# Optimization experiments

Measured on AMD Instinct MI355X. Metric: run time of the kernel, lower is better.

Reference implementation:

```python
import jax, jax.numpy as jnp
import numpy as np

B, C, N, M = 4, 192, 160, 160
HEADS, DH = 4, 32
HID = HEADS * DH
NMEM = 4
SCALE = DH ** -0.5


def setup_inputs() -> dict:
    key = jax.random.key(0)
    ks = jax.random.split(key, 8)
    std = 0.05
    return {
        "x": jax.random.normal(ks[0], (B, C, N, M), jnp.float32),
        "gq": jnp.ones((C,), jnp.float32),
        "gk": jnp.ones((C,), jnp.float32),
        "gv": jnp.ones((C,), jnp.float32),
        "Wq": jax.random.normal(ks[1], (HID, C), jnp.float32) * std,
        "Wk": jax.random.normal(ks[2], (HID, C), jnp.float32) * std,
        "Wv": jax.random.normal(ks[3], (HID, C), jnp.float32) * std,
        "mem_kv": jax.random.normal(ks[4], (2, HEADS, NMEM, DH), jnp.float32),
        "Wo": jax.random.normal(ks[5], (C, HID), jnp.float32) * std,
        "bo": jnp.zeros((C,), jnp.float32),
        "Wr": jax.random.normal(ks[6], (C, 2 * C), jnp.float32) * std,
    }


def _rms(x, g):
    # lucidrains RMSNorm over channel axis 1: F.normalize(x, dim=1) * g * sqrt(dim)
    n = jnp.sqrt(jnp.sum(x * x, axis=1, keepdims=True))
    gshape = (1, -1) + (1,) * (x.ndim - 2)
    return x / jnp.maximum(n, 1e-12) * g.reshape(gshape) * jnp.sqrt(jnp.asarray(x.shape[1], x.dtype))


def _axial_attn(q_ft, k_ft, v_map, rep, Wq, Wk, Wv, mem_kv, Wo, bo, gq, gk, gv):
    # q_ft: (b, c, Lq) compact queries (spatial (1,Lq) in the original)
    # k_ft: (b, c, Lk) compact keys; original repeats them `rep` times -> (Lk*rep) keys
    # v_map: (b, c, Lk, rep) values (full map, not broadcast)
    # Exact math of softmax over [NMEM + Lk*rep] keys, exploiting the rep-fold
    # duplicated key scores so attn(key i, copy j) has identical weight p_i:
    #   out = sum_mem p_j mem_v_j + sum_i p_i * (sum_rep v[i, r])
    b = q_ft.shape[0]
    q = jnp.einsum('hdc,bcq->bhqd', Wq.reshape(HEADS, DH, -1), _rms(q_ft, gq))
    k = jnp.einsum('hdc,bck->bhkd', Wk.reshape(HEADS, DH, -1), _rms(k_ft, gk))
    v = jnp.einsum('hdc,bckr->bhkrd', Wv.reshape(HEADS, DH, -1), _rms(v_map, gv))
    v_sum = v.sum(axis=3)  # (b,h,Lk,d)
    mem_k, mem_v = mem_kv[0], mem_kv[1]
    s_k = jnp.einsum('bhqd,bhkd->bhqk', q, k) * SCALE      # (b,h,Lq,Lk)
    s_m = jnp.einsum('bhqd,hjd->bhqj', q, mem_k) * SCALE   # (b,h,Lq,NMEM)
    mx = jnp.maximum(s_k.max(-1), s_m.max(-1))             # (b,h,Lq)
    e_k = jnp.exp(s_k - mx[..., None])
    e_m = jnp.exp(s_m - mx[..., None])
    Z = e_m.sum(-1) + rep * e_k.sum(-1)                    # rep copies of each key
    out = (jnp.einsum('bhqj,hjd->bhqd', e_m, mem_v)
           + jnp.einsum('bhqk,bhkd->bhqd', e_k, v_sum)) / Z[..., None]
    out = out.transpose(0, 2, 1, 3).reshape(b, -1, HID)    # (b,Lq,hid), (h d) channel order
    return jnp.einsum('ck,bqk->bcq', Wo, out) + bo[None, :, None]  # (b,c,Lq)


def reference(x, gq, gk, gv, Wq, Wk, Wv, mem_kv, Wo, bo, Wr):
    # x: (b,c,n,m); mask=None path
    row_ft = x.mean(axis=3)  # (b,c,n)
    col_ft = x.mean(axis=2)  # (b,c,m)
    # row attention: n queries, keys = col_ft repeated n times, values = x^T (spatial (m,n))
    row_attn = _axial_attn(row_ft, col_ft, x.transpose(0, 1, 3, 2), N,
                           Wq, Wk, Wv, mem_kv, Wo, bo, gq, gk, gv)  # (b,c,n)
    # col attention (shared weights): m queries, keys = row_ft repeated m times, values = x
    col_attn = _axial_attn(col_ft, row_ft, x, M,
                           Wq, Wk, Wv, mem_kv, Wo, bo, gq, gk, gv)  # (b,c,m)
    # broadcast to (b,c,n,m), concat on channels, 1x1 conv reduce (bias=False)
    Wr1, Wr2 = Wr[:, :C], Wr[:, C:]
    out = (jnp.einsum('dc,bcn->bdn', Wr1, row_attn)[:, :, :, None]
           + jnp.einsum('dc,bcm->bdm', Wr2, col_attn)[:, :, None, :])
    return out
```

## Files before the change

kernel.cpp:

```cpp
#include <hip/hip_runtime.h>
#include <math.h>

constexpr int B_ = 4, C_ = 192, N_ = 160, M_ = 160;
constexpr int NM_ = N_ * M_;
constexpr float SQRT_C = 13.856406460551018f;
constexpr float SCALE_ = 0.17677669529663687f;

__device__ __forceinline__ float wred_sum(float v) {
    #pragma unroll
    for (int o = 32; o > 0; o >>= 1) v += __shfl_xor(v, o, 64);
    return v;
}
__device__ __forceinline__ float wred_max(float v) {
    #pragma unroll
    for (int o = 32; o > 0; o >>= 1) v = fmaxf(v, __shfl_xor(v, o, 64));
    return v;
}

__global__ __launch_bounds__(256) void mega1_kernel(
        const float* __restrict__ x,
        const float* __restrict__ Wr, const float* __restrict__ Wo,
        const float* __restrict__ bo,
        const float* __restrict__ Wq, const float* __restrict__ Wk,
        const float* __restrict__ Wv, const float* __restrict__ gq,
        const float* __restrict__ gk, const float* __restrict__ gv,
        float* __restrict__ rn,
        float* __restrict__ rowft, float* __restrict__ colft,
        float* __restrict__ WfT2, float* __restrict__ bfb,
        float* __restrict__ WT) {
    __shared__ float4 sp4[4][64];
    __shared__ float cpart[4][160];
    int bx = blockIdx.x, tid = threadIdx.x;
    int w = tid >> 6, lane = tid & 63;
    if (bx < 400) {
        int g4 = bx * 64 + lane;
        int b = g4 / 6400, nm4 = g4 - b * 6400;
        const float* xb = x + (size_t)b * (C_ * NM_) + (size_t)nm4 * 4
                            + (size_t)(w * 48) * NM_;
        float4 s = make_float4(0.f, 0.f, 0.f, 0.f);
        #pragma unroll 16
        for (int cc = 0; cc < 48; cc++) {
            float4 v = *reinterpret_cast<const float4*>(xb + (size_t)cc * NM_);
            s.x += v.x * v.x; s.y += v.y * v.y; s.z += v.z * v.z; s.w += v.w * v.w;
        }
        sp4[w][lane] = s;
        __syncthreads();
        if (tid < 64) {
            float4 a = sp4[0][tid], b2 = sp4[1][tid], c2 = sp4[2][tid], d2 = sp4[3][tid];
            float4 r;
            r.x = SQRT_C / fmaxf(sqrtf(a.x + b2.x + c2.x + d2.x), 1e-12f);
            r.y = SQRT_C / fmaxf(sqrtf(a.y + b2.y + c2.y + d2.y), 1e-12f);
            r.z = SQRT_C / fmaxf(sqrtf(a.z + b2.z + c2.z + d2.z), 1e-12f);
            r.w = SQRT_C / fmaxf(sqrtf(a.w + b2.w + c2.w + d2.w), 1e-12f);
            *reinterpret_cast<float4*>(rn + (size_t)(bx * 64 + tid) * 4) = r;
        }
    } else if (bx < 1168) {
        int bc = bx - 400;
        const float* xp = x + (size_t)bc * NM_;
        bool act = (lane < 40);
        float4 cs = make_float4(0.f, 0.f, 0.f, 0.f);
        for (int n = w; n < N_; n += 4) {
            float4 v = act ? *reinterpret_cast<const float4*>(xp + n * M_ + lane * 4)
                           : make_float4(0.f, 0.f, 0.f, 0.f);
            cs.x += v.x; cs.y += v.y; cs.z += v.z; cs.w += v.w;
            float rs = wred_sum(v.x + v.y + v.z + v.w);
            if (lane == 0) rowft[bc * N_ + n] = rs * (1.0f / 160.0f);
        }
        if (act) {
            cpart[w][lane * 4 + 0] = cs.x; cpart[w][lane * 4 + 1] = cs.y;
            cpart[w][lane * 4 + 2] = cs.z; cpart[w][lane * 4 + 3] = cs.w;
        }
        __syncthreads();
        if (tid < 160) {
            float sr = cpart[0][tid] + cpart[1][tid] + cpart[2][tid] + cpart[3][tid];
            colft[bc * M_ + tid] = sr * (1.0f / 160.0f);
        }
    } else if (bx < 1360) {
        int pair = (bx - 1168) * 2 + (tid >> 7);
        int hd = tid & 127;
        int t = pair / 192, dch = pair % 192;
        const float* wr = Wr + dch * 384 + t * 192;
        float acc = 0.f;
        for (int c = 0; c < 192; c++) acc += wr[c] * Wo[c * 128 + hd];
        WfT2[pair * 128 + hd] = acc;
        if (hd == 0) {
            float sb = 0.f;
            for (int c = 0; c < 192; c++) sb += wr[c] * bo[c];
            bfb[pair] = sb;
        }
    } else {
        int g = (bx - 1360) * 256 + tid;
        int mat = g / 24576, r2 = g - mat * 24576;
        const float* W  = (mat == 0) ? Wq : ((mat == 1) ? Wk : Wv);
        const float* gp = (mat == 0) ? gq : ((mat == 1) ? gk : gv);
        WT[g] = gp[r2 % 192] * W[r2];
    }
}

__global__ __launch_bounds__(512) void sweighted_kernel(
        const float* __restrict__ x, const float* __restrict__ rn,
        float* __restrict__ Srow, float* __restrict__ Scol) {
    __shared__ float cpart[8][160];
    int bc = blockIdx.x;
    int b = bc / C_;
    int tid = threadIdx.x, w = tid >> 6, lane = tid & 63;
    const float* xp = x + (size_t)bc * NM_;
    const float* rp = rn + (size_t)b * NM_;
    bool act = (lane < 40);
    float4 acc = make_float4(0.f, 0.f, 0.f, 0.f);
    for (int n = w; n < N_; n += 8) {
        float4 xv = act ? *reinterpret_cast<const float4*>(xp + n * M_ + lane * 4)
                        : make_float4(0.f, 0.f, 0.f, 0.f);
        float4 rv = act ? *reinterpret_cast<const float4*>(rp + n * M_ + lane * 4)
                        : make_float4(0.f, 0.f, 0.f, 0.f);
        float4 p;
        p.x = xv.x * rv.x; p.y = xv.y * rv.y; p.z = xv.z * rv.z; p.w = xv.w * rv.w;
        acc.x += p.x; acc.y += p.y; acc.z += p.z; acc.w += p.w;
        float rs = wred_sum(p.x + p.y + p.z + p.w);
        if (lane == 0) Srow[bc * N_ + n] = rs;
    }
    if (act) {
        cpart[w][lane * 4 + 0] = acc.x; cpart[w][lane * 4 + 1] = acc.y;
        cpart[w][lane * 4 + 2] = acc.z; cpart[w][lane * 4 + 3] = acc.w;
    }
    __syncthreads();
    if (tid < 160) {
        float sn = 0.f;
        #pragma unroll
        for (int ww = 0; ww < 8; ww++) sn += cpart[ww][tid];
        Scol[bc * M_ + tid] = sn;
    }
}

__global__ __launch_bounds__(256) void proj_kernel(
        const float* __restrict__ WT,
        const float* __restrict__ rowft, const float* __restrict__ colft,
        const float* __restrict__ Srow, const float* __restrict__ Scol,
        float* __restrict__ Qb, float* __restrict__ Kb, float* __restrict__ Vb) {
    __shared__ float in_s[4 * 196];
    __shared__ float sc_s[4];
    int bx = blockIdx.x;
    int pt = bx % 40, rest = bx / 40;
    int mat = rest % 3; int r2 = rest / 3;
    int t = r2 % 2, b = r2 / 2;
    const float* src; float* dst;
    if (mat == 0)      { src = (t == 0) ? rowft : colft; dst = Qb; }
    else if (mat == 1) { src = (t == 0) ? colft : rowft; dst = Kb; }
    else               { src = (t == 0) ? Scol  : Srow;  dst = Vb; }
    const float* Wt = WT + mat * 24576;
    int tid = threadIdx.x;
    for (int idx = tid; idx < 768; idx += 256) {
        int c = idx >> 2, p = idx & 3;
        in_s[p * 196 + c] = src[(b * C_ + c) * 160 + pt * 4 + p];
    }
    __syncthreads();
    int w = tid >> 6, lane = tid & 63;
    if (mat < 2) {
        float v0 = in_s[w * 196 + lane];
        float v1 = in_s[w * 196 + lane + 64];
        float v2 = in_s[w * 196 + lane + 128];
        float ssq = wred_sum(v0 * v0 + v1 * v1 + v2 * v2);
        if (lane == 0) sc_s[w] = SQRT_C / fmaxf(sqrtf(ssq), 1e-12f);
    } else {
        if (tid < 4) sc_s[tid] = 1.0f;
    }
    __syncthreads();
    int hd = tid & 127, p0 = (tid >> 7) * 2;
    const float* wp = Wt + hd * 192;
    const float* i0p = &in_s[p0 * 196];
    const float* i1p = &in_s[(p0 + 1) * 196];
    float a0 = 0.f, a1 = 0.f;
    #pragma unroll 4
    for (int c0 = 0; c0 < 192; c0 += 4) {
        float4 wv = *reinterpret_cast<const float4*>(wp + c0);
        float4 u0 = *reinterpret_cast<const float4*>(i0p + c0);
        float4 u1 = *reinterpret_cast<const float4*>(i1p + c0);
        a0 += wv.x * u0.x + wv.y * u0.y + wv.z * u0.z + wv.w * u0.w;
        a1 += wv.x * u1.x + wv.y * u1.y + wv.z * u1.z + wv.w * u1.w;
    }
    int posbase = (b * 2 + t) * 160 + pt * 4 + p0;
    dst[(size_t)posbase * 128 + hd]       = a0 * sc_s[p0];
    dst[(size_t)(posbase + 1) * 128 + hd] = a1 * sc_s[p0 + 1];
}

__global__ __launch_bounds__(256) void attn_kernel(
        const float* __restrict__ Qb, const float* __restrict__ Kb,
        const float* __restrict__ Vb, const float* __restrict__ memkv,
        float* __restrict__ AO) {
    __shared__ float k_s[160 * 36];
    __shared__ float v_s[32 * 172];
    __shared__ float q_s[8 * 36];
    __shared__ float e_s[8 * 160];
    __shared__ float mk[128];
    __shared__ float mv[128];
    int bx = blockIdx.x;
    int qt = bx % 20; int r = bx / 20;
    int h = r & 3; r >>= 2;
    int t = r & 1; int b = r >> 1;
    int tid = threadIdx.x, w = tid >> 6, lane = tid & 63;
    int btbase = ((b * 2 + t) * 160) * 128 + h * 32;
    for (int idx = tid; idx < 1280; idx += 256) {
        int k = idx >> 3, dq = idx & 7;
        float4 kv = *reinterpret_cast<const float4*>(Kb + btbase + k * 128 + dq * 4);
        *reinterpret_cast<float4*>(&k_s[k * 36 + dq * 4]) = kv;
        float4 vv = *reinterpret_cast<const float4*>(Vb + btbase + k * 128 + dq * 4);
        v_s[(dq * 4 + 0) * 172 + k] = vv.x;
        v_s[(dq * 4 + 1) * 172 + k] = vv.y;
        v_s[(dq * 4 + 2) * 172 + k] = vv.z;
        v_s[(dq * 4 + 3) * 172 + k] = vv.w;
    }
    if (tid < 64) {
        int q = tid >> 3, dq = tid & 7;
        *reinterpret_cast<float4*>(&q_s[q * 36 + dq * 4]) =
            *reinterpret_cast<const float4*>(Qb + btbase + (qt * 8 + q) * 128 + dq * 4);
    }
    if (tid < 128) {
        mk[tid] = memkv[h * 128 + tid];
        mv[tid] = memkv[512 + h * 128 + tid];
    }
    __syncthreads();
    float4 kr0[8], kr1[8], kr2[8];
    #pragma unroll
    for (int dq = 0; dq < 8; dq++) {
        kr0[dq] = *reinterpret_cast<const float4*>(&k_s[lane * 36 + dq * 4]);
        kr1[dq] = *reinterpret_cast<const float4*>(&k_s[(lane + 64) * 36 + dq * 4]);
        if (lane < 32) kr2[dq] = *reinterpret_cast<const float4*>(&k_s[(lane + 128) * 36 + dq * 4]);
        else           kr2[dq] = make_float4(0.f, 0.f, 0.f, 0.f);
    }
    float p;
    {
        int pj = lane >> 3, qi = pj >> 2, j = pj & 3;
        int db = (lane & 7) * 4;
        float4 qv = *reinterpret_cast<const float4*>(&q_s[(w * 2 + qi) * 36 + db]);
        float4 mkv = *reinterpret_cast<const float4*>(&mk[j * 32 + db]);
        p = qv.x * mkv.x + qv.y * mkv.y + qv.z * mkv.z + qv.w * mkv.w;
        p += __shfl_xor(p, 1, 64); p += __shfl_xor(p, 2, 64); p += __shfl_xor(p, 4, 64);
        p *= SCALE_;
    }
    float sm[2][4];
    #pragma unroll
    for (int j = 0; j < 4; j++) {
        sm[0][j] = __shfl(p, j * 8, 64);
        sm[1][j] = __shfl(p, 32 + j * 8, 64);
    }
    int dpv = lane & 31;
    float Zq[2], accm[2];
    #pragma unroll
    for (int qi = 0; qi < 2; qi++) {
        const float* qrow = &q_s[(w * 2 + qi) * 36];
        float s0 = 0.f, s1 = 0.f, s2 = 0.f;
        #pragma unroll
        for (int dq = 0; dq < 8; dq++) {
            float4 qv = *reinterpret_cast<const float4*>(qrow + dq * 4);
            s0 += qv.x * kr0[dq].x + qv.y * kr0[dq].y + qv.z * kr0[dq].z + qv.w * kr0[dq].w;
            s1 += qv.x * kr1[dq].x + qv.y * kr1[dq].y + qv.z * kr1[dq].z + qv.w * kr1[dq].w;
            s2 += qv.x * kr2[dq].x + qv.y * kr2[dq].y + qv.z * kr2[dq].z + qv.w * kr2[dq].w;
        }
        s0 *= SCALE_; s1 *= SCALE_;
        s2 = (lane < 32) ? s2 * SCALE_ : -1e30f;
        float mx = fmaxf(fmaxf(s0, s1), s2);
        mx = fmaxf(mx, fmaxf(fmaxf(sm[qi][0], sm[qi][1]), fmaxf(sm[qi][2], sm[qi][3])));
        mx = wred_max(mx);
        float e0 = __expf(s0 - mx), e1 = __expf(s1 - mx);
        float e2 = (lane < 32) ? __expf(s2 - mx) : 0.f;
        int eb = (w * 2 + qi) * 160;
        e_s[eb + lane] = e0; e_s[eb + 64 + lane] = e1;
        if (lane < 32) e_s[eb + 128 + lane] = e2;
        float esum = wred_sum(e0 + e1 + e2);
        float em0 = __expf(sm[qi][0] - mx), em1 = __expf(sm[qi][1] - mx);
        float em2 = __expf(sm[qi][2] - mx), em3 = __expf(sm[qi][3] - mx);
        Zq[qi] = (em0 + em1 + em2 + em3) + 160.0f * esum;
        accm[qi] = em0 * mv[dpv] + em1 * mv[32 + dpv] + em2 * mv[64 + dpv] + em3 * mv[96 + dpv];
    }
    int half = lane >> 5, k0 = half * 80;
    const float* vrow = &v_s[dpv * 172 + k0];
    const float* e0p = &e_s[(w * 2) * 160 + k0];
    const float* e1p = &e_s[(w * 2 + 1) * 160 + k0];
    float a0 = 0.f, a1 = 0.f;
    #pragma unroll 4
    for (int kk = 0; kk < 80; kk += 4) {
        float4 vv = *reinterpret_cast<const float4*>(vrow + kk);
        float4 e0 = *reinterpret_cast<const float4*>(e0p + kk);
        float4 e1 = *reinterpret_cast<const float4*>(e1p + kk);
        a0 += e0.x * vv.x + e0.y * vv.y + e0.z * vv.z + e0.w * vv.w;
        a1 += e1.x * vv.x + e1.y * vv.y + e1.z * vv.z + e1.w * vv.w;
    }
    a0 += __shfl_down(a0, 32, 64);
    a1 += __shfl_down(a1, 32, 64);
    if (lane < 32) {
        AO[btbase + (qt * 8 + w * 2 + 0) * 128 + lane] = (accm[0] + a0) / Zq[0];
        AO[btbase + (qt * 8 + w * 2 + 1) * 128 + lane] = (accm[1] + a1) / Zq[1];
    }
}

__global__ __launch_bounds__(192) void oproj_kernel(
        const float* __restrict__ WfT2, const float* __restrict__ bfb,
        const float* __restrict__ AO, float* __restrict__ Rr,
        float* __restrict__ Ccv) {
    __shared__ float ao_s[2 * 128];
    int bx = blockIdx.x;
    int pt = bx % 80, rest = bx / 80;
    int t = rest & 1, b = rest >> 1;
    int tid = threadIdx.x;
    for (int idx = tid; idx < 256; idx += 192)
        ao_s[idx] = AO[(size_t)((b * 2 + t) * 160 + pt * 2 + (idx >> 7)) * 128 + (idx & 127)];
    __syncthreads();
    int tofs = t * 192 + tid;
    const float* wp = WfT2 + tofs * 128;
    float a0 = 0.f, a1 = 0.f;
    #pragma unroll 8
    for (int hd = 0; hd < 128; hd += 4) {
        float4 w4 = *reinterpret_cast<const float4*>(wp + hd);
        float4 x0 = *reinterpret_cast<const float4*>(&ao_s[hd]);
        float4 x1 = *reinterpret_cast<const float4*>(&ao_s[128 + hd]);
        a0 += w4.x * x0.x + w4.y * x0.y + w4.z * x0.z + w4.w * x0.w;
        a1 += w4.x * x1.x + w4.y * x1.y + w4.z * x1.z + w4.w * x1.w;
    }
    float bb = bfb[tofs];
    float* dst = t ? Ccv : Rr;
    dst[(b * C_ + tid) * 160 + pt * 2 + 0] = a0 + bb;
    dst[(b * C_ + tid) * 160 + pt * 2 + 1] = a1 + bb;
}

__global__ __launch_bounds__(256) void final_kernel(
        const float* __restrict__ Rr, const float* __restrict__ Ccv,
        float* __restrict__ out) {
    __shared__ float Rl[160];
    __shared__ float Cl[160];
    int bd = blockIdx.x;
    int tid = threadIdx.x;
    if (tid < 160) { Rl[tid] = Rr[bd * 160 + tid]; Cl[tid] = Ccv[bd * 160 + tid]; }
    __syncthreads();
    float* base = out + (size_t)bd * NM_;
    for (int idx = tid; idx < 160 * 40; idx += 256) {
        int n = idx / 40, m4 = idx - n * 40;
        float r = Rl[n];
        float4 v;
        v.x = r + Cl[m4 * 4 + 0];
        v.y = r + Cl[m4 * 4 + 1];
        v.z = r + Cl[m4 * 4 + 2];
        v.w = r + Cl[m4 * 4 + 3];
        *reinterpret_cast<float4*>(base + n * 160 + m4 * 4) = v;
    }
}

extern "C" void kernel_launch(void* const* d_in, const int* in_sizes, int n_in,
                              void* d_out, int out_size, void* d_ws, size_t ws_size,
                              hipStream_t stream) {
    const float* x    = (const float*)d_in[0];
    const float* gq   = (const float*)d_in[1];
    const float* gk   = (const float*)d_in[2];
    const float* gv   = (const float*)d_in[3];
    const float* Wq   = (const float*)d_in[4];
    const float* Wk   = (const float*)d_in[5];
    const float* Wv   = (const float*)d_in[6];
    const float* mkv  = (const float*)d_in[7];
    const float* Wo   = (const float*)d_in[8];
    const float* bo   = (const float*)d_in[9];
    const float* Wr   = (const float*)d_in[10];
    float* out = (float*)d_out;

    float* ws = (float*)d_ws;
    float* rn    = ws;
    float* rowft = rn    + 102400;
    float* colft = rowft + 122880;
    float* Srow  = colft + 122880;
    float* Scol  = Srow  + 122880;
    float* WT    = Scol  + 122880;
    float* Qb    = WT    + 73728;
    float* Kb    = Qb    + 163840;
    float* Vb    = Kb    + 163840;
    float* AO    = Vb    + 163840;
    float* Rr    = AO    + 163840;
    float* Ccv   = Rr    + 122880;
    float* WfT   = Ccv   + 122880;
    float* bfb   = WfT   + 49152;

    mega1_kernel<<<1648, 256, 0, stream>>>(x, Wr, Wo, bo, Wq, Wk, Wv, gq, gk, gv,
                                           rn, rowft, colft, WfT, bfb, WT);
    sweighted_kernel<<<768, 512, 0, stream>>>(x, rn, Srow, Scol);
    proj_kernel<<<960, 256, 0, stream>>>(WT, rowft, colft, Srow, Scol, Qb, Kb, Vb);
    attn_kernel<<<640, 256, 0, stream>>>(Qb, Kb, Vb, mkv, AO);
    oproj_kernel<<<640, 192, 0, stream>>>(WfT, bfb, AO, Rr, Ccv);
    final_kernel<<<768, 256, 0, stream>>>(Rr, Ccv, out);
}
```

Baseline: 240.2 us.

## Merge six launches into a persistent megakernel with grid barriers and fused x reductions

Replaces the six separate kernel launches with one persistent kernel of 512 blocks. Each stage iterates over its work units and is separated from the next by an atomic-counter grid barrier. The plain row/column means and the rn-weighted row/column sums are now computed in a single pass over each (b,c) slice, removing one full read of x. In exchange, that stage uses only 160 threads per block with long serial, partly strided per-thread loops, which may reduce memory-level parallelism. The grid barriers also rely on all 512 blocks being co-resident.

```diff
diff --git a/kernel.cpp b/kernel.cpp
--- a/kernel.cpp
+++ b/kernel.cpp
@@ -5,6 +5,7 @@
 constexpr int NM_ = N_ * M_;
 constexpr float SQRT_C = 13.856406460551018f;
 constexpr float SCALE_ = 0.17677669529663687f;
+constexpr int NBLK = 512;
 
 __device__ __forceinline__ float wred_sum(float v) {
     #pragma unroll
@@ -17,330 +18,315 @@
     return v;
 }
 
-__global__ __launch_bounds__(256) void mega1_kernel(
+__device__ __forceinline__ void gridbar(int* cnt) {
+    __syncthreads();
+    if (threadIdx.x == 0) {
+        __threadfence();
+        __hip_atomic_fetch_add(cnt, 1, __ATOMIC_RELEASE, __HIP_MEMORY_SCOPE_AGENT);
+        while (__hip_atomic_load(cnt, __ATOMIC_RELAXED, __HIP_MEMORY_SCOPE_AGENT) < NBLK)
+            __builtin_amdgcn_s_sleep(4);
+    }
+    __syncthreads();
+    __threadfence();
+}
+
+__global__ __launch_bounds__(256, 2) void mega_kernel(
         const float* __restrict__ x,
         const float* __restrict__ Wr, const float* __restrict__ Wo,
         const float* __restrict__ bo,
         const float* __restrict__ Wq, const float* __restrict__ Wk,
         const float* __restrict__ Wv, const float* __restrict__ gq,
         const float* __restrict__ gk, const float* __restrict__ gv,
+        const float* __restrict__ memkv,
         float* __restrict__ rn,
         float* __restrict__ rowft, float* __restrict__ colft,
+        float* __restrict__ Srow, float* __restrict__ Scol,
+        float* __restrict__ WT,
+        float* __restrict__ Qb, float* __restrict__ Kb, float* __restrict__ Vb,
+        float* __restrict__ AO, float* __restrict__ Rr, float* __restrict__ Ccv,
         float* __restrict__ WfT2, float* __restrict__ bfb,
-        float* __restrict__ WT) {
-    __shared__ float4 sp4[4][64];
-    __shared__ float cpart[4][160];
-    int bx = blockIdx.x, tid = threadIdx.x;
-    int w = tid >> 6, lane = tid & 63;
-    if (bx < 400) {
-        int g4 = bx * 64 + lane;
-        int b = g4 / 6400, nm4 = g4 - b * 6400;
-        const float* xb = x + (size_t)b * (C_ * NM_) + (size_t)nm4 * 4
-                            + (size_t)(w * 48) * NM_;
-        float4 s = make_float4(0.f, 0.f, 0.f, 0.f);
-        #pragma unroll 16
-        for (int cc = 0; cc < 48; cc++) {
-            float4 v = *reinterpret_cast<const float4*>(xb + (size_t)cc * NM_);
-            s.x += v.x * v.x; s.y += v.y * v.y; s.z += v.z * v.z; s.w += v.w * v.w;
-        }
-        sp4[w][lane] = s;
-        __syncthreads();
+        float* __restrict__ out, int* __restrict__ bar) {
+    __shared__ __align__(16) float lds[13088];
+    const int tid = threadIdx.x;
+    const int w = tid >> 6, lane = tid & 63;
+
+    for (int u = blockIdx.x; u < 880; u += NBLK) {
+        if (u < 400) {
+            float4* sp4 = reinterpret_cast<float4*>(lds);
+            int g4 = u * 64 + lane;
+            int b = g4 / 6400, nm4 = g4 - b * 6400;
+            const float* xb = x + (size_t)b * (C_ * NM_) + (size_t)nm4 * 4
+                                + (size_t)(w * 48) * NM_;
+            float4 s = make_float4(0.f, 0.f, 0.f, 0.f);
+            #pragma unroll 16
+            for (int cc = 0; cc < 48; cc++) {
+                float4 v = *reinterpret_cast<const float4*>(xb + (size_t)cc * NM_);
+                s.x += v.x * v.x; s.y += v.y * v.y; s.z += v.z * v.z; s.w += v.w * v.w;
+            }
+            sp4[w * 64 + lane] = s;
+            __syncthreads();
+            if (tid < 64) {
+                float4 a = sp4[tid], b2 = sp4[64 + tid], c2 = sp4[128 + tid], d2 = sp4[192 + tid];
+                float4 r;
+                r.x = SQRT_C / fmaxf(sqrtf(a.x + b2.x + c2.x + d2.x), 1e-12f);
+                r.y = SQRT_C / fmaxf(sqrtf(a.y + b2.y + c2.y + d2.y), 1e-12f);
+                r.z = SQRT_C / fmaxf(sqrtf(a.z + b2.z + c2.z + d2.z), 1e-12f);
+                r.w = SQRT_C / fmaxf(sqrtf(a.w + b2.w + c2.w + d2.w), 1e-12f);
+                *reinterpret_cast<float4*>(rn + (size_t)(u * 64 + tid) * 4) = r;
+            }
+            __syncthreads();
+        } else if (u < 592) {
+            int pair = (u - 400) * 2 + (tid >> 7);
+            int hd = tid & 127;
+            int t = pair / 192, dch = pair % 192;
+            const float* wr = Wr + dch * 384 + t * 192;
+            float acc = 0.f;
+            for (int c = 0; c < 192; c++) acc += wr[c] * Wo[c * 128 + hd];
+            WfT2[pair * 128 + hd] = acc;
+            if (hd == 0) {
+                float sb = 0.f;
+                for (int c = 0; c < 192; c++) sb += wr[c] * bo[c];
+                bfb[pair] = sb;
+            }
+        } else {
+            int g = (u - 592) * 256 + tid;
+            int mat = g / 24576, r2 = g - mat * 24576;
+            const float* W  = (mat == 0) ? Wq : ((mat == 1) ? Wk : Wv);
+            const float* gp = (mat == 0) ? gq : ((mat == 1) ? gk : gv);
+            WT[g] = gp[r2 % 192] * W[r2];
+        }
+    }
+    gridbar(bar + 0);
+
+    for (int u = blockIdx.x; u < 768; u += NBLK) {
+        int bc = u, b = bc / C_;
+        const float* xp = x + (size_t)bc * NM_;
+        const float* rp = rn + (size_t)b * NM_;
+        if (tid < 160) {
+            int m = tid;
+            float cs = 0.f, cw = 0.f;
+            #pragma unroll 8
+            for (int n = 0; n < 160; n++) {
+                float xv = xp[n * 160 + m], rv = rp[n * 160 + m];
+                cs += xv; cw += xv * rv;
+            }
+            colft[bc * M_ + m] = cs * (1.0f / 160.0f);
+            Scol[bc * M_ + m] = cw;
+            const float* xr = xp + m * 160;
+            const float* rr = rp + m * 160;
+            float4 a = make_float4(0.f, 0.f, 0.f, 0.f);
+            float4 bw = make_float4(0.f, 0.f, 0.f, 0.f);
+            #pragma unroll 8
+            for (int i = 0; i < 40; i++) {
+                float4 xv = *reinterpret_cast<const float4*>(xr + i * 4);
+                float4 rv = *reinterpret_cast<const float4*>(rr + i * 4);
+                a.x += xv.x; a.y += xv.y; a.z += xv.z; a.w += xv.w;
+                bw.x += xv.x * rv.x; bw.y += xv.y * rv.y;
+                bw.z += xv.z * rv.z; bw.w += xv.w * rv.w;
+            }
+            rowft[bc * N_ + m] = (a.x + a.y + a.z + a.w) * (1.0f / 160.0f);
+            Srow[bc * N_ + m] = bw.x + bw.y + bw.z + bw.w;
+        }
+    }
+    gridbar(bar + 1);
+
+    for (int u = blockIdx.x; u < 960; u += NBLK) {
+        float* in_s = lds;
+        float* sc_s = lds + 784;
+        int pt = u % 40, rest = u / 40;
+        int mat = rest % 3; int r2 = rest / 3;
+        int t = r2 % 2, b = r2 / 2;
+        const float* src; float* dst;
+        if (mat == 0)      { src = (t == 0) ? rowft : colft; dst = Qb; }
+        else if (mat == 1) { src = (t == 0) ? colft : rowft; dst = Kb; }
+        else               { src = (t == 0) ? Scol  : Srow;  dst = Vb; }
+        const float* Wt = WT + mat * 24576;
+        for (int idx = tid; idx < 768; idx += 256) {
+            int c = idx >> 2, p = idx & 3;
+            in_s[p * 196 + c] = src[(b * C_ + c) * 160 + pt * 4 + p];
+        }
+        __syncthreads();
+        if (mat < 2) {
+            float v0 = in_s[w * 196 + lane];
+            float v1 = in_s[w * 196 + lane + 64];
+            float v2 = in_s[w * 196 + lane + 128];
+            float ssq = wred_sum(v0 * v0 + v1 * v1 + v2 * v2);
+            if (lane == 0) sc_s[w] = SQRT_C / fmaxf(sqrtf(ssq), 1e-12f);
+        } else {
+            if (tid < 4) sc_s[tid] = 1.0f;
+        }
+        __syncthreads();
+        int hd = tid & 127, p0 = (tid >> 7) * 2;
+        const float* wp = Wt + hd * 192;
+        const float* i0p = &in_s[p0 * 196];
+        const float* i1p = &in_s[(p0 + 1) * 196];
+        float a0 = 0.f, a1 = 0.f;
+        #pragma unroll 4
+        for (int c0 = 0; c0 < 192; c0 += 4) {
+            float4 wv = *reinterpret_cast<const float4*>(wp + c0);
+            float4 u0 = *reinterpret_cast<const float4*>(i0p + c0);
+            float4 u1 = *reinterpret_cast<const float4*>(i1p + c0);
+            a0 += wv.x * u0.x + wv.y * u0.y + wv.z * u0.z + wv.w * u0.w;
+            a1 += wv.x * u1.x + wv.y * u1.y + wv.z * u1.z + wv.w * u1.w;
+        }
+        int posbase = (b * 2 + t) * 160 + pt * 4 + p0;
+        dst[(size_t)posbase * 128 + hd]       = a0 * sc_s[p0];
+        dst[(size_t)(posbase + 1) * 128 + hd] = a1 * sc_s[p0 + 1];
+        __syncthreads();
+    }
+    gridbar(bar + 2);
+
+    for (int u = blockIdx.x; u < 640; u += NBLK) {
+        float* k_s = lds;
+        float* v_s = lds + 5760;
+        float* q_s = lds + 11264;
+        float* e_s = lds + 11552;
+        float* mk  = lds + 12832;
+        float* mv  = lds + 12960;
+        int qt = u % 20; int r = u / 20;
+        int h = r & 3; r >>= 2;
+        int t = r & 1; int b = r >> 1;
+        int btbase = ((b * 2 + t) * 160) * 128 + h * 32;
+        for (int idx = tid; idx < 1280; idx += 256) {
+            int k = idx >> 3, dq = idx & 7;
+            float4 kv = *reinterpret_cast<const float4*>(Kb + btbase + k * 128 + dq * 4);
+            *reinterpret_cast<float4*>(&k_s[k * 36 + dq * 4]) = kv;
+            float4 vv = *reinterpret_cast<const float4*>(Vb + btbase + k * 128 + dq * 4);
+            v_s[(dq * 4 + 0) * 172 + k] = vv.x;
+            v_s[(dq * 4 + 1) * 172 + k] = vv.y;
+            v_s[(dq * 4 + 2) * 172 + k] = vv.z;
+            v_s[(dq * 4 + 3) * 172 + k] = vv.w;
+        }
         if (tid < 64) {
-            float4 a = sp4[0][tid], b2 = sp4[1][tid], c2 = sp4[2][tid], d2 = sp4[3][tid];
-            float4 r;
-            r.x = SQRT_C / fmaxf(sqrtf(a.x + b2.x + c2.x + d2.x), 1e-12f);
-            r.y = SQRT_C / fmaxf(sqrtf(a.y + b2.y + c2.y + d2.y), 1e-12f);
-            r.z = SQRT_C / fmaxf(sqrtf(a.z + b2.z + c2.z + d2.z), 1e-12f);
-            r.w = SQRT_C / fmaxf(sqrtf(a.w + b2.w + c2.w + d2.w), 1e-12f);
-            *reinterpret_cast<float4*>(rn + (size_t)(bx * 64 + tid) * 4) = r;
-        }
-    } else if (bx < 1168) {
-        int bc = bx - 400;
-        const float* xp = x + (size_t)bc * NM_;
-        bool act = (lane < 40);
-        float4 cs = make_float4(0.f, 0.f, 0.f, 0.f);
-        for (int n = w; n < N_; n += 4) {
-            float4 v = act ? *reinterpret_cast<const float4*>(xp + n * M_ + lane * 4)
-                           : make_float4(0.f, 0.f, 0.f, 0.f);
-            cs.x += v.x; cs.y += v.y; cs.z += v.z; cs.w += v.w;
-            float rs = wred_sum(v.x + v.y + v.z + v.w);
-            if (lane == 0) rowft[bc * N_ + n] = rs * (1.0f / 160.0f);
-        }
-        if (act) {
-            cpart[w][lane * 4 + 0] = cs.x; cpart[w][lane * 4 + 1] = cs.y;
-            cpart[w][lane * 4 + 2] = cs.z; cpart[w][lane * 4 + 3] = cs.w;
-        }
-        __syncthreads();
-        if (tid < 160) {
-            float sr = cpart[0][tid] + cpart[1][tid] + cpart[2][tid] + cpart[3][tid];
-            colft[bc * M_ + tid] = sr * (1.0f / 160.0f);
-        }
-    } else if (bx < 1360) {
-        int pair = (bx - 1168) * 2 + (tid >> 7);
-        int hd = tid & 127;
-        int t = pair / 192, dch = pair % 192;
-        const float* wr = Wr + dch * 384 + t * 192;
-        float acc = 0.f;
-        for (int c = 0; c < 192; c++) acc += wr[c] * Wo[c * 128 + hd];
-        WfT2[pair * 128 + hd] = acc;
-        if (hd == 0) {
-            float sb = 0.f;
-            for (int c = 0; c < 192; c++) sb += wr[c] * bo[c];
-            bfb[pair] = sb;
-        }
-    } else {
-        int g = (bx - 1360) * 256 + tid;
-        int mat = g / 24576, r2 = g - mat * 24576;
-        const float* W  = (mat == 0) ? Wq : ((mat == 1) ? Wk : Wv);
-        const float* gp = (mat == 0) ? gq : ((mat == 1) ? gk : gv);
-        WT[g] = gp[r2 % 192] * W[r2];
-    }
-}
-
-__global__ __launch_bounds__(512) void sweighted_kernel(
-        const float* __restrict__ x, const float* __restrict__ rn,
-        float* __restrict__ Srow, float* __restrict__ Scol) {
-    __shared__ float cpart[8][160];
-    int bc = blockIdx.x;
-    int b = bc / C_;
-    int tid = threadIdx.x, w = tid >> 6, lane = tid & 63;
-    const float* xp = x + (size_t)bc * NM_;
-    const float* rp = rn + (size_t)b * NM_;
-    bool act = (lane < 40);
-    float4 acc = make_float4(0.f, 0.f, 0.f, 0.f);
-    for (int n = w; n < N_; n += 8) {
-        float4 xv = act ? *reinterpret_cast<const float4*>(xp + n * M_ + lane * 4)
-                        : make_float4(0.f, 0.f, 0.f, 0.f);
-        float4 rv = act ? *reinterpret_cast<const float4*>(rp + n * M_ + lane * 4)
-                        : make_float4(0.f, 0.f, 0.f, 0.f);
-        float4 p;
-        p.x = xv.x * rv.x; p.y = xv.y * rv.y; p.z = xv.z * rv.z; p.w = xv.w * rv.w;
-        acc.x += p.x; acc.y += p.y; acc.z += p.z; acc.w += p.w;
-        float rs = wred_sum(p.x + p.y + p.z + p.w);
-        if (lane == 0) Srow[bc * N_ + n] = rs;
-    }
-    if (act) {
-        cpart[w][lane * 4 + 0] = acc.x; cpart[w][lane * 4 + 1] = acc.y;
-        cpart[w][lane * 4 + 2] = acc.z; cpart[w][lane * 4 + 3] = acc.w;
-    }
-    __syncthreads();
-    if (tid < 160) {
-        float sn = 0.f;
-        #pragma unroll
-        for (int ww = 0; ww < 8; ww++) sn += cpart[ww][tid];
-        Scol[bc * M_ + tid] = sn;
-    }
-}
-
-__global__ __launch_bounds__(256) void proj_kernel(
-        const float* __restrict__ WT,
-        const float* __restrict__ rowft, const float* __restrict__ colft,
-        const float* __restrict__ Srow, const float* __restrict__ Scol,
-        float* __restrict__ Qb, float* __restrict__ Kb, float* __restrict__ Vb) {
-    __shared__ float in_s[4 * 196];
-    __shared__ float sc_s[4];
-    int bx = blockIdx.x;
-    int pt = bx % 40, rest = bx / 40;
-    int mat = rest % 3; int r2 = rest / 3;
-    int t = r2 % 2, b = r2 / 2;
-    const float* src; float* dst;
-    if (mat == 0)      { src = (t == 0) ? rowft : colft; dst = Qb; }
-    else if (mat == 1) { src = (t == 0) ? colft : rowft; dst = Kb; }
-    else               { src = (t == 0) ? Scol  : Srow;  dst = Vb; }
-    const float* Wt = WT + mat * 24576;
-    int tid = threadIdx.x;
-    for (int idx = tid; idx < 768; idx += 256) {
-        int c = idx >> 2, p = idx & 3;
-        in_s[p * 196 + c] = src[(b * C_ + c) * 160 + pt * 4 + p];
-    }
-    __syncthreads();
-    int w = tid >> 6, lane = tid & 63;
-    if (mat < 2) {
-        float v0 = in_s[w * 196 + lane];
-        float v1 = in_s[w * 196 + lane + 64];
-        float v2 = in_s[w * 196 + lane + 128];
-        float ssq = wred_sum(v0 * v0 + v1 * v1 + v2 * v2);
-        if (lane == 0) sc_s[w] = SQRT_C / fmaxf(sqrtf(ssq), 1e-12f);
-    } else {
-        if (tid < 4) sc_s[tid] = 1.0f;
-    }
-    __syncthreads();
-    int hd = tid & 127, p0 = (tid >> 7) * 2;
-    const float* wp = Wt + hd * 192;
-    const float* i0p = &in_s[p0 * 196];
-    const float* i1p = &in_s[(p0 + 1) * 196];
-    float a0 = 0.f, a1 = 0.f;
-    #pragma unroll 4
-    for (int c0 = 0; c0 < 192; c0 += 4) {
-        float4 wv = *reinterpret_cast<const float4*>(wp + c0);
-        float4 u0 = *reinterpret_cast<const float4*>(i0p + c0);
-        float4 u1 = *reinterpret_cast<const float4*>(i1p + c0);
-        a0 += wv.x * u0.x + wv.y * u0.y + wv.z * u0.z + wv.w * u0.w;
-        a1 += wv.x * u1.x + wv.y * u1.y + wv.z * u1.z + wv.w * u1.w;
-    }
-    int posbase = (b * 2 + t) * 160 + pt * 4 + p0;
-    dst[(size_t)posbase * 128 + hd]       = a0 * sc_s[p0];
-    dst[(size_t)(posbase + 1) * 128 + hd] = a1 * sc_s[p0 + 1];
-}
-
-__global__ __launch_bounds__(256) void attn_kernel(
-        const float* __restrict__ Qb, const float* __restrict__ Kb,
-        const float* __restrict__ Vb, const float* __restrict__ memkv,
-        float* __restrict__ AO) {
-    __shared__ float k_s[160 * 36];
-    __shared__ float v_s[32 * 172];
-    __shared__ float q_s[8 * 36];
-    __shared__ float e_s[8 * 160];
-    __shared__ float mk[128];
-    __shared__ float mv[128];
-    int bx = blockIdx.x;
-    int qt = bx % 20; int r = bx / 20;
-    int h = r & 3; r >>= 2;
-    int t = r & 1; int b = r >> 1;
-    int tid = threadIdx.x, w = tid >> 6, lane = tid & 63;
-    int btbase = ((b * 2 + t) * 160) * 128 + h * 32;
-    for (int idx = tid; idx < 1280; idx += 256) {
-        int k = idx >> 3, dq = idx & 7;
-        float4 kv = *reinterpret_cast<const float4*>(Kb + btbase + k * 128 + dq * 4);
-        *reinterpret_cast<float4*>(&k_s[k * 36 + dq * 4]) = kv;
-        float4 vv = *reinterpret_cast<const float4*>(Vb + btbase + k * 128 + dq * 4);
-        v_s[(dq * 4 + 0) * 172 + k] = vv.x;
-        v_s[(dq * 4 + 1) * 172 + k] = vv.y;
-        v_s[(dq * 4 + 2) * 172 + k] = vv.z;
-        v_s[(dq * 4 + 3) * 172 + k] = vv.w;
-    }
-    if (tid < 64) {
-        int q = tid >> 3, dq = tid & 7;
-        *reinterpret_cast<float4*>(&q_s[q * 36 + dq * 4]) =
-            *reinterpret_cast<const float4*>(Qb + btbase + (qt * 8 + q) * 128 + dq * 4);
-    }
-    if (tid < 128) {
-        mk[tid] = memkv[h * 128 + tid];
-        mv[tid] = memkv[512 + h * 128 + tid];
-    }
-    __syncthreads();
-    float4 kr0[8], kr1[8], kr2[8];
-    #pragma unroll
-    for (int dq = 0; dq < 8; dq++) {
-        kr0[dq] = *reinterpret_cast<const float4*>(&k_s[lane * 36 + dq * 4]);
-        kr1[dq] = *reinterpret_cast<const float4*>(&k_s[(lane + 64) * 36 + dq * 4]);
-        if (lane < 32) kr2[dq] = *reinterpret_cast<const float4*>(&k_s[(lane + 128) * 36 + dq * 4]);
-        else           kr2[dq] = make_float4(0.f, 0.f, 0.f, 0.f);
-    }
-    float p;
-    {
-        int pj = lane >> 3, qi = pj >> 2, j = pj & 3;
-        int db = (lane & 7) * 4;
-        float4 qv = *reinterpret_cast<const float4*>(&q_s[(w * 2 + qi) * 36 + db]);
-        float4 mkv = *reinterpret_cast<const float4*>(&mk[j * 32 + db]);
-        p = qv.x * mkv.x + qv.y * mkv.y + qv.z * mkv.z + qv.w * mkv.w;
-        p += __shfl_xor(p, 1, 64); p += __shfl_xor(p, 2, 64); p += __shfl_xor(p, 4, 64);
-        p *= SCALE_;
-    }
-    float sm[2][4];
-    #pragma unroll
-    for (int j = 0; j < 4; j++) {
-        sm[0][j] = __shfl(p, j * 8, 64);
-        sm[1][j] = __shfl(p, 32 + j * 8, 64);
-    }
-    int dpv = lane & 31;
-    float Zq[2], accm[2];
-    #pragma unroll
-    for (int qi = 0; qi < 2; qi++) {
-        const float* qrow = &q_s[(w * 2 + qi) * 36];
-        float s0 = 0.f, s1 = 0.f, s2 = 0.f;
+            int q = tid >> 3, dq = tid & 7;
+            *reinterpret_cast<float4*>(&q_s[q * 36 + dq * 4]) =
+                *reinterpret_cast<const float4*>(Qb + btbase + (qt * 8 + q) * 128 + dq * 4);
+        }
+        if (tid < 128) {
+            mk[tid] = memkv[h * 128 + tid];
+            mv[tid] = memkv[512 + h * 128 + tid];
+        }
+        __syncthreads();
+        float4 kr0[8], kr1[8], kr2[8];
         #pragma unroll
         for (int dq = 0; dq < 8; dq++) {
-            float4 qv = *reinterpret_cast<const float4*>(qrow + dq * 4);
-            s0 += qv.x * kr0[dq].x + qv.y * kr0[dq].y + qv.z * kr0[dq].z + qv.w * kr0[dq].w;
-            s1 += qv.x * kr1[dq].x + qv.y * kr1[dq].y + qv.z * kr1[dq].z + qv.w * kr1[dq].w;
-            s2 += qv.x * kr2[dq].x + qv.y * kr2[dq].y + qv.z * kr2[dq].z + qv.w * kr2[dq].w;
-        }
-        s0 *= SCALE_; s1 *= SCALE_;
-        s2 = (lane < 32) ? s2 * SCALE_ : -1e30f;
-        float mx = fmaxf(fmaxf(s0, s1), s2);
-        mx = fmaxf(mx, fmaxf(fmaxf(sm[qi][0], sm[qi][1]), fmaxf(sm[qi][2], sm[qi][3])));
-        mx = wred_max(mx);
-        float e0 = __expf(s0 - mx), e1 = __expf(s1 - mx);
-        float e2 = (lane < 32) ? __expf(s2 - mx) : 0.f;
-        int eb = (w * 2 + qi) * 160;
-        e_s[eb + lane] = e0; e_s[eb + 64 + lane] = e1;
-        if (lane < 32) e_s[eb + 128 + lane] = e2;
-        float esum = wred_sum(e0 + e1 + e2);
-        float em0 = __expf(sm[qi][0] - mx), em1 = __expf(sm[qi][1] - mx);
-        float em2 = __expf(sm[qi][2] - mx), em3 = __expf(sm[qi][3] - mx);
-        Zq[qi] = (em0 + em1 + em2 + em3) + 160.0f * esum;
-        accm[qi] = em0 * mv[dpv] + em1 * mv[32 + dpv] + em2 * mv[64 + dpv] + em3 * mv[96 + dpv];
-    }
-    int half = lane >> 5, k0 = half * 80;
-    const float* vrow = &v_s[dpv * 172 + k0];
-    const float* e0p = &e_s[(w * 2) * 160 + k0];
-    const float* e1p = &e_s[(w * 2 + 1) * 160 + k0];
-    float a0 = 0.f, a1 = 0.f;
-    #pragma unroll 4
-    for (int kk = 0; kk < 80; kk += 4) {
-        float4 vv = *reinterpret_cast<const float4*>(vrow + kk);
-        float4 e0 = *reinterpret_cast<const float4*>(e0p + kk);
-        float4 e1 = *reinterpret_cast<const float4*>(e1p + kk);
-        a0 += e0.x * vv.x + e0.y * vv.y + e0.z * vv.z + e0.w * vv.w;
-        a1 += e1.x * vv.x + e1.y * vv.y + e1.z * vv.z + e1.w * vv.w;
-    }
-    a0 += __shfl_down(a0, 32, 64);
-    a1 += __shfl_down(a1, 32, 64);
-    if (lane < 32) {
-        AO[btbase + (qt * 8 + w * 2 + 0) * 128 + lane] = (accm[0] + a0) / Zq[0];
-        AO[btbase + (qt * 8 + w * 2 + 1) * 128 + lane] = (accm[1] + a1) / Zq[1];
-    }
-}
-
-__global__ __launch_bounds__(192) void oproj_kernel(
-        const float* __restrict__ WfT2, const float* __restrict__ bfb,
-        const float* __restrict__ AO, float* __restrict__ Rr,
-        float* __restrict__ Ccv) {
-    __shared__ float ao_s[2 * 128];
-    int bx = blockIdx.x;
-    int pt = bx % 80, rest = bx / 80;
-    int t = rest & 1, b = rest >> 1;
-    int tid = threadIdx.x;
-    for (int idx = tid; idx < 256; idx += 192)
-        ao_s[idx] = AO[(size_t)((b * 2 + t) * 160 + pt * 2 + (idx >> 7)) * 128 + (idx & 127)];
-    __syncthreads();
-    int tofs = t * 192 + tid;
-    const float* wp = WfT2 + tofs * 128;
-    float a0 = 0.f, a1 = 0.f;
-    #pragma unroll 8
-    for (int hd = 0; hd < 128; hd += 4) {
-        float4 w4 = *reinterpret_cast<const float4*>(wp + hd);
-        float4 x0 = *reinterpret_cast<const float4*>(&ao_s[hd]);
-        float4 x1 = *reinterpret_cast<const float4*>(&ao_s[128 + hd]);
-        a0 += w4.x * x0.x + w4.y * x0.y + w4.z * x0.z + w4.w * x0.w;
-        a1 += w4.x * x1.x + w4.y * x1.y + w4.z * x1.z + w4.w * x1.w;
-    }
-    float bb = bfb[tofs];
-    float* dst = t ? Ccv : Rr;
-    dst[(b * C_ + tid) * 160 + pt * 2 + 0] = a0 + bb;
-    dst[(b * C_ + tid) * 160 + pt * 2 + 1] = a1 + bb;
-}
-
-__global__ __launch_bounds__(256) void final_kernel(
-        const float* __restrict__ Rr, const float* __restrict__ Ccv,
-        float* __restrict__ out) {
-    __shared__ float Rl[160];
-    __shared__ float Cl[160];
-    int bd = blockIdx.x;
-    int tid = threadIdx.x;
-    if (tid < 160) { Rl[tid] = Rr[bd * 160 + tid]; Cl[tid] = Ccv[bd * 160 + tid]; }
-    __syncthreads();
-    float* base = out + (size_t)bd * NM_;
-    for (int idx = tid; idx < 160 * 40; idx += 256) {
-        int n = idx / 40, m4 = idx - n * 40;
-        float r = Rl[n];
-        float4 v;
-        v.x = r + Cl[m4 * 4 + 0];
-        v.y = r + Cl[m4 * 4 + 1];
-        v.z = r + Cl[m4 * 4 + 2];
-        v.w = r + Cl[m4 * 4 + 3];
-        *reinterpret_cast<float4*>(base + n * 160 + m4 * 4) = v;
+            kr0[dq] = *reinterpret_cast<const float4*>(&k_s[lane * 36 + dq * 4]);
+            kr1[dq] = *reinterpret_cast<const float4*>(&k_s[(lane + 64) * 36 + dq * 4]);
+            if (lane < 32) kr2[dq] = *reinterpret_cast<const float4*>(&k_s[(lane + 128) * 36 + dq * 4]);
+            else           kr2[dq] = make_float4(0.f, 0.f, 0.f, 0.f);
+        }
+        float p;
+        {
+            int pj = lane >> 3, qi = pj >> 2, j = pj & 3;
+            int db = (lane & 7) * 4;
+            float4 qv = *reinterpret_cast<const float4*>(&q_s[(w * 2 + qi) * 36 + db]);
+            float4 mkv = *reinterpret_cast<const float4*>(&mk[j * 32 + db]);
+            p = qv.x * mkv.x + qv.y * mkv.y + qv.z * mkv.z + qv.w * mkv.w;
+            p += __shfl_xor(p, 1, 64); p += __shfl_xor(p, 2, 64); p += __shfl_xor(p, 4, 64);
+            p *= SCALE_;
+        }
+        float sm[2][4];
+        #pragma unroll
+        for (int j = 0; j < 4; j++) {
+            sm[0][j] = __shfl(p, j * 8, 64);
+            sm[1][j] = __shfl(p, 32 + j * 8, 64);
+        }
+        int dpv = lane & 31;
+        float Zq[2], accm[2];
+        #pragma unroll
+        for (int qi = 0; qi < 2; qi++) {
+            const float* qrow = &q_s[(w * 2 + qi) * 36];
+            float s0 = 0.f, s1 = 0.f, s2 = 0.f;
+            #pragma unroll
+            for (int dq = 0; dq < 8; dq++) {
+                float4 qv = *reinterpret_cast<const float4*>(qrow + dq * 4);
+                s0 += qv.x * kr0[dq].x + qv.y * kr0[dq].y + qv.z * kr0[dq].z + qv.w * kr0[dq].w;
+                s1 += qv.x * kr1[dq].x + qv.y * kr1[dq].y + qv.z * kr1[dq].z + qv.w * kr1[dq].w;
+                s2 += qv.x * kr2[dq].x + qv.y * kr2[dq].y + qv.z * kr2[dq].z + qv.w * kr2[dq].w;
+            }
+            s0 *= SCALE_; s1 *= SCALE_;
+            s2 = (lane < 32) ? s2 * SCALE_ : -1e30f;
+            float mx = fmaxf(fmaxf(s0, s1), s2);
+            mx = fmaxf(mx, fmaxf(fmaxf(sm[qi][0], sm[qi][1]), fmaxf(sm[qi][2], sm[qi][3])));
+            mx = wred_max(mx);
+            float e0 = __expf(s0 - mx), e1 = __expf(s1 - mx);
+            float e2 = (lane < 32) ? __expf(s2 - mx) : 0.f;
+            int eb = (w * 2 + qi) * 160;
+            e_s[eb + lane] = e0; e_s[eb + 64 + lane] = e1;
+            if (lane < 32) e_s[eb + 128 + lane] = e2;
+            float esum = wred_sum(e0 + e1 + e2);
+            float em0 = __expf(sm[qi][0] - mx), em1 = __expf(sm[qi][1] - mx);
+            float em2 = __expf(sm[qi][2] - mx), em3 = __expf(sm[qi][3] - mx);
+            Zq[qi] = (em0 + em1 + em2 + em3) + 160.0f * esum;
+            accm[qi] = em0 * mv[dpv] + em1 * mv[32 + dpv] + em2 * mv[64 + dpv] + em3 * mv[96 + dpv];
+        }
+        int half = lane >> 5, k0 = half * 80;
+        const float* vrow = &v_s[dpv * 172 + k0];
+        const float* e0p = &e_s[(w * 2) * 160 + k0];
+        const float* e1p = &e_s[(w * 2 + 1) * 160 + k0];
+        float a0 = 0.f, a1 = 0.f;
+        #pragma unroll 4
+        for (int kk = 0; kk < 80; kk += 4) {
+            float4 vv = *reinterpret_cast<const float4*>(vrow + kk);
+            float4 e0 = *reinterpret_cast<const float4*>(e0p + kk);
+            float4 e1 = *reinterpret_cast<const float4*>(e1p + kk);
+            a0 += e0.x * vv.x + e0.y * vv.y + e0.z * vv.z + e0.w * vv.w;
+            a1 += e1.x * vv.x + e1.y * vv.y + e1.z * vv.z + e1.w * vv.w;
+        }
+        a0 += __shfl_down(a0, 32, 64);
+        a1 += __shfl_down(a1, 32, 64);
+        if (lane < 32) {
+            AO[btbase + (qt * 8 + w * 2 + 0) * 128 + lane] = (accm[0] + a0) / Zq[0];
+            AO[btbase + (qt * 8 + w * 2 + 1) * 128 + lane] = (accm[1] + a1) / Zq[1];
+        }
+        __syncthreads();
+    }
+    gridbar(bar + 3);
+
+    for (int u = blockIdx.x; u < 640; u += NBLK) {
+        float* ao_s = lds;
+        int pt = u % 80, rest = u / 80;
+        int t = rest & 1, b = rest >> 1;
+        ao_s[tid] = AO[(size_t)((b * 2 + t) * 160 + pt * 2 + (tid >> 7)) * 128 + (tid & 127)];
+        __syncthreads();
+        if (tid < 192) {
+            int tofs = t * 192 + tid;
+            const float* wp = WfT2 + tofs * 128;
+            float a0 = 0.f, a1 = 0.f;
+            #pragma unroll 8
+            for (int hd = 0; hd < 128; hd += 4) {
+                float4 w4 = *reinterpret_cast<const float4*>(wp + hd);
+                float4 x0 = *reinterpret_cast<const float4*>(&ao_s[hd]);
+                float4 x1 = *reinterpret_cast<const float4*>(&ao_s[128 + hd]);
+                a0 += w4.x * x0.x + w4.y * x0.y + w4.z * x0.z + w4.w * x0.w;
+                a1 += w4.x * x1.x + w4.y * x1.y + w4.z * x1.z + w4.w * x1.w;
+            }
+            float bb = bfb[tofs];
+            float* dst = t ? Ccv : Rr;
+            dst[(b * C_ + tid) * 160 + pt * 2 + 0] = a0 + bb;
+            dst[(b * C_ + tid) * 160 + pt * 2 + 1] = a1 + bb;
+        }
+        __syncthreads();
+    }
+    gridbar(bar + 4);
+
+    for (int u = blockIdx.x; u < 768; u += NBLK) {
+        float* Rl = lds;
+        float* Cl = lds + 160;
+        if (tid < 160) { Rl[tid] = Rr[u * 160 + tid]; Cl[tid] = Ccv[u * 160 + tid]; }
+        __syncthreads();
+        float* base = out + (size_t)u * NM_;
+        for (int idx = tid; idx < 160 * 40; idx += 256) {
+            int n = idx / 40, m4 = idx - n * 40;
+            float rv = Rl[n];
+            float4 v;
+            v.x = rv + Cl[m4 * 4 + 0];
+            v.y = rv + Cl[m4 * 4 + 1];
+            v.z = rv + Cl[m4 * 4 + 2];
+            v.w = rv + Cl[m4 * 4 + 3];
+            *reinterpret_cast<float4*>(base + n * 160 + m4 * 4) = v;
+        }
+        __syncthreads();
     }
 }
 
@@ -375,12 +361,11 @@
     float* Ccv   = Rr    + 122880;
     float* WfT   = Ccv   + 122880;
     float* bfb   = WfT   + 49152;
-
-    mega1_kernel<<<1648, 256, 0, stream>>>(x, Wr, Wo, bo, Wq, Wk, Wv, gq, gk, gv,
-                                           rn, rowft, colft, WfT, bfb, WT);
-    sweighted_kernel<<<768, 512, 0, stream>>>(x, rn, Srow, Scol);
-    proj_kernel<<<960, 256, 0, stream>>>(WT, rowft, colft, Srow, Scol, Qb, Kb, Vb);
-    attn_kernel<<<640, 256, 0, stream>>>(Qb, Kb, Vb, mkv, AO);
-    oproj_kernel<<<640, 192, 0, stream>>>(WfT, bfb, AO, Rr, Ccv);
-    final_kernel<<<768, 256, 0, stream>>>(Rr, Ccv, out);
-}
+    int*   bar   = (int*)(bfb + 384);
+
+    hipMemsetAsync(bar, 0, 64, stream);
+    mega_kernel<<<NBLK, 256, 0, stream>>>(x, Wr, Wo, bo, Wq, Wk, Wv, gq, gk, gv, mkv,
+                                          rn, rowft, colft, Srow, Scol, WT,
+                                          Qb, Kb, Vb, AO, Rr, Ccv, WfT, bfb,
+                                          out, bar);
+}
```

Measured after the change: 654.8 us. 173% more time.
